# Performance work log

Hardware: AMD Instinct MI355X
Metric: run time of the kernel (lower is better)

The kernel has to match this reference:

```python
import jax, jax.numpy as jnp
import numpy as np

B, T_V, T_T, C, H = 4, 8192, 77, 1024, 16
D = C // H  # head_dim = 64


def setup_inputs() -> dict:
    key = jax.random.key(0)
    ks = jax.random.split(key, 6)
    s = 1.0 / np.sqrt(C)
    return {
        "video_features": jax.random.normal(ks[0], (B, T_V, C), jnp.float32),
        "text_features": jax.random.normal(ks[1], (B, T_T, C), jnp.float32),
        "Wq": jax.random.normal(ks[2], (C, C), jnp.float32) * s,
        "Wk": jax.random.normal(ks[3], (C, C), jnp.float32) * s,
        "Wv": jax.random.normal(ks[4], (C, C), jnp.float32) * s,
        "Wo": jax.random.normal(ks[5], (C, C), jnp.float32) * s,
    }


def reference(video_features, text_features, Wq, Wk, Wv, Wo):
    # nn.Linear(no bias): y = x @ W.T
    q = (video_features @ Wq.T).reshape(B, T_V, H, D).transpose(0, 2, 1, 3)  # [B,H,Tv,D]
    k = (text_features @ Wk.T).reshape(B, T_T, H, D).transpose(0, 2, 1, 3)   # [B,H,Tt,D]
    v = (text_features @ Wv.T).reshape(B, T_T, H, D).transpose(0, 2, 1, 3)   # [B,H,Tt,D]
    scores = jnp.einsum("bhqd,bhkd->bhqk", q, k) / jnp.sqrt(jnp.float32(D))
    attn = jax.nn.softmax(scores, axis=-1)
    out = jnp.einsum("bhqk,bhkd->bhqd", attn, v)
    out = out.transpose(0, 2, 1, 3).reshape(B, T_V, C)
    return out @ Wo.T
```

## Files before the change

kernel.cpp:

```cpp
#include <hip/hip_runtime.h>
#include <hip/hip_bf16.h>


typedef __attribute__((ext_vector_type(8))) short bf16x8;
typedef __attribute__((ext_vector_type(4))) float f32x4;
typedef __attribute__((ext_vector_type(8))) unsigned short u16x8;
typedef __attribute__((ext_vector_type(4))) unsigned short u16x4;

typedef const __attribute__((address_space(1))) void gv_t;
typedef __attribute__((address_space(3))) void lv_t;

static __device__ __forceinline__ unsigned short f2bf(float f) {
    union { float f; unsigned u; } v; v.f = f;
    unsigned r = v.u + 0x7FFFu + ((v.u >> 16) & 1u);
    return (unsigned short)(r >> 16);
}

constexpr int Bn = 4, TVn = 8192, TTn = 77, Cn = 1024, Hn = 16;

__device__ __forceinline__ void cvt8_body(const float* __restrict__ in,
                                          unsigned short* __restrict__ out, int i) {
    const float4* p = reinterpret_cast<const float4*>(in) + (size_t)i * 2;
    float4 a = p[0], b = p[1];
    u16x8 o = { f2bf(a.x), f2bf(a.y), f2bf(a.z), f2bf(a.w),
                f2bf(b.x), f2bf(b.y), f2bf(b.z), f2bf(b.w) };
    *reinterpret_cast<u16x8*>(out + (size_t)i * 8) = o;
}

__global__ __launch_bounds__(256)
void k_prep(const float* __restrict__ video, const float* __restrict__ text,
            const float* __restrict__ Wq, const float* __restrict__ Wk,
            const float* __restrict__ Wv, const float* __restrict__ Wo,
            unsigned short* __restrict__ wq_b, unsigned short* __restrict__ wo_b,
            unsigned short* __restrict__ kbuf, unsigned short* __restrict__ vbuf,
            unsigned short* __restrict__ vid_b) {
    __shared__ unsigned short As[128 * 32];
    __shared__ unsigned short Bs[128 * 32];
    const int tid = threadIdx.x;
    int bid = blockIdx.x;

    if (bid >= 48) {
        bid -= 48;
        if (bid < 512)       cvt8_body(Wq, wq_b, bid * 256 + tid);
        else if (bid < 1024) cvt8_body(Wo, wo_b, (bid - 512) * 256 + tid);
        else                 cvt8_body(video, vid_b, (bid - 1024) * 256 + tid);
        return;
    }
    const int bx = bid % 3, by = (bid / 3) % 8, bz = bid / 24;
    const float* W = bz ? Wv : Wk;
    unsigned short* out = bz ? vbuf : kbuf;
    const int M = Bn * TTn;
    const int lane = tid & 63, wv = tid >> 6;
    const int m0 = bx * 128, n0 = by * 128;
    const int wr = (wv >> 1) * 64, wc = (wv & 1) * 64;
    const int lr = lane & 15, lk = (lane >> 4) * 8, lg = lane >> 4;
    const int srow = tid >> 3, sc4 = (tid & 7) * 4;
    f32x4 acc[4][4] = {};

    float4 a0[4], b0[4], a1[4], b1[4];

#define KV_LOAD(kk, ra, rb)                                                            \
    {                                                                                  \
        _Pragma("unroll")                                                              \
        for (int it = 0; it < 4; ++it) {                                               \
            int row = it * 32 + srow;                                                  \
            int gr = m0 + row;                                                         \
            ra[it] = make_float4(0.f, 0.f, 0.f, 0.f);                                  \
            if (gr < M) ra[it] = *reinterpret_cast<const float4*>(                     \
                text + (size_t)gr * 1024 + (kk) + sc4);                                \
            rb[it] = *reinterpret_cast<const float4*>(                                 \
                W + (size_t)(n0 + row) * 1024 + (kk) + sc4);                           \
        }                                                                              \
    }

#define KV_WRITE(ra, rb)                                                               \
    {                                                                                  \
        _Pragma("unroll")                                                              \
        for (int it = 0; it < 4; ++it) {                                               \
            int row = it * 32 + srow;                                                  \
            u16x4 oa = { f2bf(ra[it].x), f2bf(ra[it].y), f2bf(ra[it].z), f2bf(ra[it].w) }; \
            *reinterpret_cast<u16x4*>(&As[row * 32 + sc4]) = oa;                       \
            u16x4 ob = { f2bf(rb[it].x), f2bf(rb[it].y), f2bf(rb[it].z), f2bf(rb[it].w) }; \
            *reinterpret_cast<u16x4*>(&Bs[row * 32 + sc4]) = ob;                       \
        }                                                                              \
    }

#define KV_COMPUTE()                                                                   \
    {                                                                                  \
        bf16x8 af[4], bfv[4];                                                          \
        _Pragma("unroll")                                                              \
        for (int m = 0; m < 4; ++m)                                                    \
            af[m] = *reinterpret_cast<const bf16x8*>(&As[(wr + m * 16 + lr) * 32 + lk]); \
        _Pragma("unroll")                                                              \
        for (int n = 0; n < 4; ++n)                                                    \
            bfv[n] = *reinterpret_cast<const bf16x8*>(&Bs[(wc + n * 16 + lr) * 32 + lk]); \
        _Pragma("unroll")                                                              \
        for (int m = 0; m < 4; ++m)                                                    \
            _Pragma("unroll")                                                          \
            for (int n = 0; n < 4; ++n)                                                \
                acc[m][n] = __builtin_amdgcn_mfma_f32_16x16x32_bf16(af[m], bfv[n], acc[m][n], 0, 0, 0); \
    }

    KV_LOAD(0, a0, b0);
    for (int kk = 0; kk < 1024; kk += 64) {
        __syncthreads();
        KV_WRITE(a0, b0);
        if (kk + 32 < 1024) KV_LOAD(kk + 32, a1, b1);
        __syncthreads();
        KV_COMPUTE();
        __syncthreads();
        KV_WRITE(a1, b1);
        if (kk + 64 < 1024) KV_LOAD(kk + 64, a0, b0);
        __syncthreads();
        KV_COMPUTE();
    }
#undef KV_LOAD
#undef KV_WRITE
#undef KV_COMPUTE

    #pragma unroll
    for (int m = 0; m < 4; ++m)
        #pragma unroll
        for (int n = 0; n < 4; ++n)
            #pragma unroll
            for (int r = 0; r < 4; ++r) {
                int grow = m0 + wr + m * 16 + lg * 4 + r;
                if (grow < M) {
                    int gcol = n0 + wc + n * 16 + lr;
                    out[(size_t)grow * 1024 + gcol] = f2bf(acc[m][n][r]);
                }
            }
}

__device__ __forceinline__ void stage_h(const unsigned short* __restrict__ src, int grow0, int kcol0,
                                        unsigned short* lds, int tid) {
    #pragma unroll
    for (int j = 0; j < 2; ++j) {
        const int row = j * 64 + (tid >> 3);
        const int sseg = (tid & 7) ^ (row & 7);
        const unsigned short* g = src + (size_t)(grow0 + row) * 1024 + kcol0 + sseg * 8;
        unsigned short* d = lds + j * 4096 + (tid >> 6) * 512;
        __builtin_amdgcn_global_load_lds((gv_t*)g, (lv_t*)d, 16, 0, 0);
    }
}

template<int BUF, int MQ>
__device__ __forceinline__ void p8_loadA(bf16x8 (&af)[4][2],
        const unsigned short (&As)[2][2][128][64], int wm, int lr, int lg) {
    #pragma unroll
    for (int m4 = 0; m4 < 4; ++m4)
        #pragma unroll
        for (int kk = 0; kk < 2; ++kk) {
            const int rl = MQ * 64 + m4 * 16 + lr;
            af[m4][kk] = *reinterpret_cast<const bf16x8*>(
                &As[BUF][wm][rl][((kk * 4 + lg) ^ (rl & 7)) * 8]);
        }
}

template<int BUF, int NQ>
__device__ __forceinline__ void p8_loadB(bf16x8 (&bg)[2][2],
        const unsigned short (&Bs)[2][2][128][64], int wn, int lr, int lg) {
    #pragma unroll
    for (int n2 = 0; n2 < 2; ++n2)
        #pragma unroll
        for (int kk = 0; kk < 2; ++kk) {
            const int nrow = wn * 64 + (NQ * 2 + n2) * 16 + lr;
            bg[n2][kk] = *reinterpret_cast<const bf16x8*>(
                &Bs[BUF][nrow >> 7][nrow & 127][((kk * 4 + lg) ^ (nrow & 7)) * 8]);
        }
}

template<int MQ, int NQ>
__device__ __forceinline__ void p8_mfma(f32x4 (&acc)[8][4],
        const bf16x8 (&af)[4][2], const bf16x8 (&bg)[2][2]) {
    #pragma unroll
    for (int m4 = 0; m4 < 4; ++m4)
        #pragma unroll
        for (int n2 = 0; n2 < 2; ++n2)
            #pragma unroll
            for (int kk = 0; kk < 2; ++kk)
                acc[MQ * 4 + m4][NQ * 2 + n2] = __builtin_amdgcn_mfma_f32_16x16x32_bf16(
                    af[m4][kk], bg[n2][kk], acc[MQ * 4 + m4][NQ * 2 + n2], 0, 0, 0);
}

#define P8_PRE()                                              \
    __builtin_amdgcn_s_barrier();                             \
    __builtin_amdgcn_s_setprio(1);

template<int OUT_MODE>
__global__ __launch_bounds__(512, 1)
void k_g256p8(const unsigned short* __restrict__ A, const unsigned short* __restrict__ Wb,
              void* __restrict__ outp) {
    __shared__ unsigned short As[2][2][128][64];
    __shared__ unsigned short Bs[2][2][128][64];
    const int tid = threadIdx.x, lane = tid & 63;
    const int wid = tid >> 6, wm = wid >> 2, wn = wid & 3;
    const int orig = blockIdx.x;
    const int work = (orig & 7) * 64 + (orig >> 3);
    const int m0 = (work >> 2) * 256, n0 = (work & 3) * 256;
    const int lr = lane & 15, lg = lane >> 4;

    f32x4 acc[8][4] = {};
    bf16x8 af[4][2], bg0[2][2], bg1[2][2];

    stage_h(A,  m0,       0,  &As[0][0][0][0], tid);
    stage_h(A,  m0 + 128, 0,  &As[0][1][0][0], tid);
    stage_h(Wb, n0,       0,  &Bs[0][0][0][0], tid);
    stage_h(Wb, n0 + 128, 0,  &Bs[0][1][0][0], tid);
    stage_h(Wb, n0,       64, &Bs[1][0][0][0], tid);
    stage_h(Wb, n0 + 128, 64, &Bs[1][1][0][0], tid);
    asm volatile("s_waitcnt vmcnt(4)" ::: "memory");
    __builtin_amdgcn_s_barrier();

    for (int t = 0; t < 16; t += 2) {
        const int k1 = (t + 1) * 64;
        const bool s2 = (t + 2) < 16, s3 = (t + 3) < 16;
        p8_loadA<0, 0>(af, As, wm, lr, lg);
        p8_loadB<0, 0>(bg0, Bs, wn, lr, lg);
        stage_h(A, m0, k1, &As[1][0][0][0], tid);
        P8_PRE(); p8_mfma<0, 0>(acc, af, bg0);
        __builtin_amdgcn_s_setprio(0); __builtin_amdgcn_s_barrier();
        p8_loadB<0, 1>(bg1, Bs, wn, lr, lg);
        stage_h(A, m0 + 128, k1, &As[1][1][0][0], tid);
        P8_PRE(); p8_mfma<0, 1>(acc, af, bg1);
        __builtin_amdgcn_s_setprio(0); __builtin_amdgcn_s_barrier();
        p8_loadA<0, 1>(af, As, wm, lr, lg);
        if (s2) stage_h(Wb, n0, k1 + 64, &Bs[0][0][0][0], tid);
        P8_PRE(); p8_mfma<1, 1>(acc, af, bg1);
        __builtin_amdgcn_s_setprio(0); __builtin_amdgcn_s_barrier();
        if (s2) stage_h(Wb, n0 + 128, k1 + 64, &Bs[0][1][0][0], tid);
        P8_PRE(); p8_mfma<1, 0>(acc, af, bg0);
        __builtin_amdgcn_s_setprio(0);
        if (s2) { asm volatile("s_waitcnt vmcnt(4)" ::: "memory"); }
        else    { asm volatile("s_waitcnt vmcnt(0)" ::: "memory"); }
        __builtin_amdgcn_s_barrier();
        p8_loadA<1, 0>(af, As, wm, lr, lg);
        p8_loadB<1, 0>(bg0, Bs, wn, lr, lg);
        if (s2) stage_h(A, m0, k1 + 64, &As[0][0][0][0], tid);
        P8_PRE(); p8_mfma<0, 0>(acc, af, bg0);
        __builtin_amdgcn_s_setprio(0); __builtin_amdgcn_s_barrier();
        p8_loadB<1, 1>(bg1, Bs, wn, lr, lg);
        if (s2) stage_h(A, m0 + 128, k1 + 64, &As[0][1][0][0], tid);
        P8_PRE(); p8_mfma<0, 1>(acc, af, bg1);
        __builtin_amdgcn_s_setprio(0); __builtin_amdgcn_s_barrier();
        p8_loadA<1, 1>(af, As, wm, lr, lg);
        if (s3) stage_h(Wb, n0, k1 + 128, &Bs[1][0][0][0], tid);
        P8_PRE(); p8_mfma<1, 1>(acc, af, bg1);
        __builtin_amdgcn_s_setprio(0); __builtin_amdgcn_s_barrier();
        if (s3) stage_h(Wb, n0 + 128, k1 + 128, &Bs[1][1][0][0], tid);
        P8_PRE(); p8_mfma<1, 0>(acc, af, bg0);
        __builtin_amdgcn_s_setprio(0);
        if (s3) { asm volatile("s_waitcnt vmcnt(4)" ::: "memory"); }
        else    { asm volatile("s_waitcnt vmcnt(0)" ::: "memory"); }
        __builtin_amdgcn_s_barrier();
    }

    #pragma unroll
    for (int mf = 0; mf < 8; ++mf)
        #pragma unroll
        for (int nf = 0; nf < 4; ++nf)
            #pragma unroll
            for (int r = 0; r < 4; ++r) {
                int grow = m0 + wm * 128 + mf * 16 + lg * 4 + r;
                int gcol = n0 + wn * 64 + nf * 16 + lr;
                if (OUT_MODE == 0) {
                    float v = acc[mf][nf][r];
                    float o = __shfl_xor(v, 1);
                    if (!(lane & 1)) {
                        float* out = (float*)outp;
                        float2 pv; pv.x = v; pv.y = o;
                        *reinterpret_cast<float2*>(out + (size_t)grow * 1024 + gcol) = pv;
                    }
                } else {
                    unsigned short bv = f2bf(acc[mf][nf][r]);
                    unsigned ov = __shfl_xor((unsigned)bv, 1);
                    if (!(lane & 1)) {
                        unsigned short* out = (unsigned short*)outp;
                        size_t off = (OUT_MODE == 1)
                            ? (size_t)grow * 1024 + gcol
                            : ((size_t)(gcol >> 6) * (Bn * TVn) + grow) * 64 + (gcol & 63);
                        *reinterpret_cast<unsigned*>(out + off) = (unsigned)bv | (ov << 16);
                    }
                }
            }
}

__global__ __launch_bounds__(512)
void k_attn5(const unsigned short* __restrict__ qh,
             const unsigned short* __restrict__ kb,
             const unsigned short* __restrict__ vb,
             unsigned short* __restrict__ aout) {
    constexpr int VP = 104;
    __shared__ unsigned short vt_s[64 * VP];
    const int tid = threadIdx.x, lane = tid & 63, wv = tid >> 6;
    const int m0 = blockIdx.x * 256;
    const int h = blockIdx.y, b = blockIdx.z;
    const size_t qhbase = ((size_t)h * (Bn * TVn) + (size_t)b * TVn + m0) * 64;
    const size_t kvbase = (size_t)b * TTn * Cn + h * 64;
    const int lr = lane & 15, lg = lane >> 4;

    for (int li = tid; li < 640; li += 512) {
        int t = li >> 3, sg = li & 7;
        u16x8 v = {0, 0, 0, 0, 0, 0, 0, 0};
        if (t < 77) v = *reinterpret_cast<const u16x8*>(vb + kvbase + (size_t)t * Cn + sg * 8);
        #pragma unroll
        for (int i = 0; i < 8; ++i) vt_s[(sg * 8 + i) * VP + t] = v[i];
    }
    for (int li = tid; li < 1024; li += 512) {
        int d = li >> 4, t = 80 + (li & 15);
        vt_s[d * VP + t] = 0;
    }

    f32x4 sc[2][5] = {};
    #pragma unroll
    for (int ks = 0; ks < 2; ++ks) {
        bf16x8 qa[2], kf[5];
        #pragma unroll
        for (int mf = 0; mf < 2; ++mf)
            qa[mf] = *reinterpret_cast<const bf16x8*>(
                qh + qhbase + (size_t)(wv * 32 + mf * 16 + lr) * 64 + ks * 32 + lg * 8);
        #pragma unroll
        for (int nf = 0; nf < 5; ++nf) {
            int t = nf * 16 + lr; if (t > 76) t = 76;
            kf[nf] = *reinterpret_cast<const bf16x8*>(
                kb + kvbase + (size_t)t * Cn + ks * 32 + lg * 8);
        }
        #pragma unroll
        for (int mf = 0; mf < 2; ++mf)
            #pragma unroll
            for (int nf = 0; nf < 5; ++nf)
                sc[mf][nf] = __builtin_amdgcn_mfma_f32_16x16x32_bf16(kf[nf], qa[mf], sc[mf][nf], 0, 0, 0);
    }

    unsigned pk[2][6][2];
    constexpr float CEXP = 0.125f * 1.44269504088896340736f;
    #pragma unroll
    for (int mf = 0; mf < 2; ++mf) {
        float mx = -1e30f;
        #pragma unroll
        for (int nf = 0; nf < 5; ++nf)
            #pragma unroll
            for (int r = 0; r < 4; ++r)
                if (!(nf == 4 && r >= 1)) mx = fmaxf(mx, sc[mf][nf][r]);
                else if (lg != 3)         mx = fmaxf(mx, sc[mf][nf][r]);
        mx = fmaxf(mx, __shfl_xor(mx, 16));
        mx = fmaxf(mx, __shfl_xor(mx, 32));
        float p[5][4];
        float sum = 0.f;
        #pragma unroll
        for (int nf = 0; nf < 5; ++nf)
            #pragma unroll
            for (int r = 0; r < 4; ++r) {
                bool valid = !(nf == 4 && lg == 3 && r >= 1);
                float pv = valid ? exp2f((sc[mf][nf][r] - mx) * CEXP) : 0.f;
                p[nf][r] = pv;
                sum += pv;
            }
        sum += __shfl_xor(sum, 16);
        sum += __shfl_xor(sum, 32);
        float inv = 1.f / sum;
        #pragma unroll
        for (int nf = 0; nf < 5; ++nf) {
            pk[mf][nf][0] = (unsigned)f2bf(p[nf][0] * inv) | ((unsigned)f2bf(p[nf][1] * inv) << 16);
            pk[mf][nf][1] = (unsigned)f2bf(p[nf][2] * inv) | ((unsigned)f2bf(p[nf][3] * inv) << 16);
        }
        pk[mf][5][0] = 0; pk[mf][5][1] = 0;
    }

    __syncthreads();

    f32x4 ovv[2][4] = {};
    const int sel = lg >> 1;
    const int srcA = ((lg & 1) * 2) * 16 + lr;
    const int srcB = ((lg & 1) * 2 + 1) * 16 + lr;
    #pragma unroll
    for (int ks = 0; ks < 3; ++ks) {
        bf16x8 vf[4];
        #pragma unroll
        for (int nf = 0; nf < 4; ++nf)
            vf[nf] = *reinterpret_cast<const bf16x8*>(
                &vt_s[(nf * 16 + lr) * VP + ks * 32 + lg * 8]);
        #pragma unroll
        for (int mf = 0; mf < 2; ++mf) {
            unsigned w0l = __shfl(pk[mf][ks * 2 + 0][0], srcA);
            unsigned w0h = __shfl(pk[mf][ks * 2 + 1][0], srcA);
            unsigned w1l = __shfl(pk[mf][ks * 2 + 0][1], srcA);
            unsigned w1h = __shfl(pk[mf][ks * 2 + 1][1], srcA);
            unsigned w2l = __shfl(pk[mf][ks * 2 + 0][0], srcB);
            unsigned w2h = __shfl(pk[mf][ks * 2 + 1][0], srcB);
            unsigned w3l = __shfl(pk[mf][ks * 2 + 0][1], srcB);
            unsigned w3h = __shfl(pk[mf][ks * 2 + 1][1], srcB);
            union { uint4 u; bf16x8 v; } pa;
            pa.u.x = sel ? w0h : w0l;
            pa.u.y = sel ? w1h : w1l;
            pa.u.z = sel ? w2h : w2l;
            pa.u.w = sel ? w3h : w3l;
            #pragma unroll
            for (int nf = 0; nf < 4; ++nf)
                ovv[mf][nf] = __builtin_amdgcn_mfma_f32_16x16x32_bf16(pa.v, vf[nf], ovv[mf][nf], 0, 0, 0);
        }
    }

    #pragma unroll
    for (int mf = 0; mf < 2; ++mf)
        #pragma unroll
        for (int nf = 0; nf < 4; ++nf)
            #pragma unroll
            for (int r = 0; r < 4; ++r) {
                unsigned short bv = f2bf(ovv[mf][nf][r]);
                unsigned o = __shfl_xor((unsigned)bv, 1);
                if (!(lane & 1)) {
                    int row = m0 + wv * 32 + mf * 16 + lg * 4 + r;
                    int col = h * 64 + nf * 16 + lr;
                    *reinterpret_cast<unsigned*>(aout + ((size_t)b * TVn + row) * Cn + col) =
                        (unsigned)bv | (o << 16);
                }
            }
}

extern "C" void kernel_launch(void* const* d_in, const int* in_sizes, int n_in,
                              void* d_out, int out_size, void* d_ws, size_t ws_size,
                              hipStream_t stream) {
    const float* video = (const float*)d_in[0];
    const float* text  = (const float*)d_in[1];
    const float* Wq = (const float*)d_in[2];
    const float* Wk = (const float*)d_in[3];
    const float* Wv = (const float*)d_in[4];
    const float* Wo = (const float*)d_in[5];
    float* out = (float*)d_out;

    char* ws = (char*)d_ws;
    unsigned short* wq_b  = (unsigned short*)(ws);
    unsigned short* wo_b  = (unsigned short*)(ws + (2u << 20));
    unsigned short* kbuf  = (unsigned short*)(ws + (4u << 20));
    unsigned short* vbuf  = (unsigned short*)(ws + (5u << 20));
    unsigned short* qhbuf = (unsigned short*)(ws + (6u << 20));
    unsigned short* vid_b = (unsigned short*)(ws + (70u << 20));

    k_prep<<<48 + 512 + 512 + 16384, 256, 0, stream>>>(
        video, text, Wq, Wk, Wv, Wo, wq_b, wo_b, kbuf, vbuf, vid_b);

    k_g256p8<2><<<512, 512, 0, stream>>>(vid_b, wq_b, (void*)qhbuf);

    dim3 ga(TVn / 256, Hn, Bn);
    k_attn5<<<ga, 512, 0, stream>>>(qhbuf, kbuf, vbuf, vid_b);

    k_g256p8<0><<<512, 512, 0, stream>>>(vid_b, wo_b, (void*)out);
}
```

Baseline: 255.4 us.

## Fuse video fp32-to-bf16 conversion into Q projection GEMM A-operand load

Removes the separate conversion of video features to bf16 in the prep kernel and instead loads fp32 video tiles directly in a new Q-projection GEMM, converting to bf16 in registers before writing to LDS with an XOR swizzle. This eliminates writing and rereading a large bf16 intermediate buffer. In exchange, the GEMM reads twice the bytes per A tile (fp32), repeated across the N-tile blocks, and holds extra prefetch registers.

```diff
diff --git a/kernel.cpp b/kernel.cpp
--- a/kernel.cpp
+++ b/kernel.cpp
@@ -28,12 +28,11 @@
 }
 
 __global__ __launch_bounds__(256)
-void k_prep(const float* __restrict__ video, const float* __restrict__ text,
+void k_prep(const float* __restrict__ text,
             const float* __restrict__ Wq, const float* __restrict__ Wk,
             const float* __restrict__ Wv, const float* __restrict__ Wo,
             unsigned short* __restrict__ wq_b, unsigned short* __restrict__ wo_b,
-            unsigned short* __restrict__ kbuf, unsigned short* __restrict__ vbuf,
-            unsigned short* __restrict__ vid_b) {
+            unsigned short* __restrict__ kbuf, unsigned short* __restrict__ vbuf) {
     __shared__ unsigned short As[128 * 32];
     __shared__ unsigned short Bs[128 * 32];
     const int tid = threadIdx.x;
@@ -41,9 +40,8 @@
 
     if (bid >= 48) {
         bid -= 48;
-        if (bid < 512)       cvt8_body(Wq, wq_b, bid * 256 + tid);
-        else if (bid < 1024) cvt8_body(Wo, wo_b, (bid - 512) * 256 + tid);
-        else                 cvt8_body(video, vid_b, (bid - 1024) * 256 + tid);
+        if (bid < 512) cvt8_body(Wq, wq_b, bid * 256 + tid);
+        else           cvt8_body(Wo, wo_b, (bid - 512) * 256 + tid);
         return;
     }
     const int bx = bid % 3, by = (bid / 3) % 8, bz = bid / 24;
@@ -186,6 +184,120 @@
 #define P8_PRE()                                              \
     __builtin_amdgcn_s_barrier();                             \
     __builtin_amdgcn_s_setprio(1);
+
+__global__ __launch_bounds__(512, 1)
+void k_gq_fused(const float* __restrict__ A, const unsigned short* __restrict__ Wb,
+                unsigned short* __restrict__ outp) {
+    __shared__ unsigned short As[2][2][128][64];
+    __shared__ unsigned short Bs[2][2][128][64];
+    const int tid = threadIdx.x, lane = tid & 63;
+    const int wid = tid >> 6, wm = wid >> 2, wn = wid & 3;
+    const int orig = blockIdx.x;
+    const int work = (orig & 7) * 64 + (orig >> 3);
+    const int m0 = (work >> 2) * 256, n0 = (work & 3) * 256;
+    const int lr = lane & 15, lg = lane >> 4;
+    const int srow = tid >> 3, sw = tid & 7, sa = (tid & 7) ^ ((tid >> 3) & 7);
+
+    f32x4 acc[8][4] = {};
+    bf16x8 af[4][2], bg0[2][2], bg1[2][2];
+    float4 ra0[2][2][2], ra1[2][2][2];
+
+#define AQ_LOAD(bank, kt)                                                          \
+    { const int kc_ = (kt) * 64;                                                   \
+      _Pragma("unroll") for (int hh = 0; hh < 2; ++hh)                             \
+      _Pragma("unroll") for (int j = 0; j < 2; ++j) {                              \
+          const float* g_ = A + (size_t)(m0 + hh * 128 + j * 64 + srow) * 1024 + kc_ + sa * 8; \
+          bank[hh][j][0] = *reinterpret_cast<const float4*>(g_);                   \
+          bank[hh][j][1] = *reinterpret_cast<const float4*>(g_ + 4);               \
+      } }
+
+#define AQ_WRITE(bank, BUF, HH)                                                    \
+    { _Pragma("unroll") for (int j = 0; j < 2; ++j) {                              \
+          float4 u_ = bank[HH][j][0], v_ = bank[HH][j][1];                         \
+          u16x8 o_ = { f2bf(u_.x), f2bf(u_.y), f2bf(u_.z), f2bf(u_.w),             \
+                       f2bf(v_.x), f2bf(v_.y), f2bf(v_.z), f2bf(v_.w) };           \
+          *reinterpret_cast<u16x8*>(&As[BUF][HH][j * 64 + srow][sw * 8]) = o_;     \
+      } }
+
+    AQ_LOAD(ra0, 0);
+    AQ_LOAD(ra1, 1);
+    stage_h(Wb, n0,       0,  &Bs[0][0][0][0], tid);
+    stage_h(Wb, n0 + 128, 0,  &Bs[0][1][0][0], tid);
+    stage_h(Wb, n0,       64, &Bs[1][0][0][0], tid);
+    stage_h(Wb, n0 + 128, 64, &Bs[1][1][0][0], tid);
+    AQ_WRITE(ra0, 0, 0);
+    AQ_WRITE(ra0, 0, 1);
+    asm volatile("s_waitcnt vmcnt(4)" ::: "memory");
+    asm volatile("s_waitcnt lgkmcnt(0)" ::: "memory");
+    __builtin_amdgcn_s_barrier();
+
+    for (int t = 0; t < 16; t += 2) {
+        const int k1 = (t + 1) * 64;
+        const bool s2 = (t + 2) < 16, s3 = (t + 3) < 16;
+        p8_loadA<0, 0>(af, As, wm, lr, lg);
+        p8_loadB<0, 0>(bg0, Bs, wn, lr, lg);
+        AQ_WRITE(ra1, 1, 0);
+        if (s2) AQ_LOAD(ra0, t + 2);
+        P8_PRE(); p8_mfma<0, 0>(acc, af, bg0);
+        __builtin_amdgcn_s_setprio(0); __builtin_amdgcn_s_barrier();
+        p8_loadB<0, 1>(bg1, Bs, wn, lr, lg);
+        AQ_WRITE(ra1, 1, 1);
+        P8_PRE(); p8_mfma<0, 1>(acc, af, bg1);
+        __builtin_amdgcn_s_setprio(0);
+        asm volatile("s_waitcnt lgkmcnt(0)" ::: "memory");
+        __builtin_amdgcn_s_barrier();
+        p8_loadA<0, 1>(af, As, wm, lr, lg);
+        if (s2) stage_h(Wb, n0, k1 + 64, &Bs[0][0][0][0], tid);
+        P8_PRE(); p8_mfma<1, 1>(acc, af, bg1);
+        __builtin_amdgcn_s_setprio(0); __builtin_amdgcn_s_barrier();
+        if (s2) stage_h(Wb, n0 + 128, k1 + 64, &Bs[0][1][0][0], tid);
+        P8_PRE(); p8_mfma<1, 0>(acc, af, bg0);
+        __builtin_amdgcn_s_setprio(0);
+        if (s2) { asm volatile("s_waitcnt vmcnt(4)" ::: "memory"); }
+        else    { asm volatile("s_waitcnt vmcnt(0)" ::: "memory"); }
+        __builtin_amdgcn_s_barrier();
+        p8_loadA<1, 0>(af, As, wm, lr, lg);
+        p8_loadB<1, 0>(bg0, Bs, wn, lr, lg);
+        if (s2) AQ_WRITE(ra0, 0, 0);
+        if (s3) AQ_LOAD(ra1, t + 3);
+        P8_PRE(); p8_mfma<0, 0>(acc, af, bg0);
+        __builtin_amdgcn_s_setprio(0); __builtin_amdgcn_s_barrier();
+        p8_loadB<1, 1>(bg1, Bs, wn, lr, lg);
+        if (s2) AQ_WRITE(ra0, 0, 1);
+        P8_PRE(); p8_mfma<0, 1>(acc, af, bg1);
+        __builtin_amdgcn_s_setprio(0);
+        asm volatile("s_waitcnt lgkmcnt(0)" ::: "memory");
+        __builtin_amdgcn_s_barrier();
+        p8_loadA<1, 1>(af, As, wm, lr, lg);
+        if (s3) stage_h(Wb, n0, k1 + 128, &Bs[1][0][0][0], tid);
+        P8_PRE(); p8_mfma<1, 1>(acc, af, bg1);
+        __builtin_amdgcn_s_setprio(0); __builtin_amdgcn_s_barrier();
+        if (s3) stage_h(Wb, n0 + 128, k1 + 128, &Bs[1][1][0][0], tid);
+        P8_PRE(); p8_mfma<1, 0>(acc, af, bg0);
+        __builtin_amdgcn_s_setprio(0);
+        if (s3) { asm volatile("s_waitcnt vmcnt(4)" ::: "memory"); }
+        else    { asm volatile("s_waitcnt vmcnt(0)" ::: "memory"); }
+        __builtin_amdgcn_s_barrier();
+    }
+#undef AQ_LOAD
+#undef AQ_WRITE
+
+    #pragma unroll
+    for (int mf = 0; mf < 8; ++mf)
+        #pragma unroll
+        for (int nf = 0; nf < 4; ++nf)
+            #pragma unroll
+            for (int r = 0; r < 4; ++r) {
+                int grow = m0 + wm * 128 + mf * 16 + lg * 4 + r;
+                int gcol = n0 + wn * 64 + nf * 16 + lr;
+                unsigned short bv = f2bf(acc[mf][nf][r]);
+                unsigned ov = __shfl_xor((unsigned)bv, 1);
+                if (!(lane & 1)) {
+                    size_t off = ((size_t)(gcol >> 6) * (Bn * TVn) + grow) * 64 + (gcol & 63);
+                    *reinterpret_cast<unsigned*>(outp + off) = (unsigned)bv | (ov << 16);
+                }
+            }
+}
 
 template<int OUT_MODE>
 __global__ __launch_bounds__(512, 1)
@@ -435,15 +547,15 @@
     unsigned short* kbuf  = (unsigned short*)(ws + (4u << 20));
     unsigned short* vbuf  = (unsigned short*)(ws + (5u << 20));
     unsigned short* qhbuf = (unsigned short*)(ws + (6u << 20));
-    unsigned short* vid_b = (unsigned short*)(ws + (70u << 20));
-
-    k_prep<<<48 + 512 + 512 + 16384, 256, 0, stream>>>(
-        video, text, Wq, Wk, Wv, Wo, wq_b, wo_b, kbuf, vbuf, vid_b);
-
-    k_g256p8<2><<<512, 512, 0, stream>>>(vid_b, wq_b, (void*)qhbuf);
+    unsigned short* abuf  = (unsigned short*)(ws + (70u << 20));
+
+    k_prep<<<48 + 512 + 512, 256, 0, stream>>>(
+        text, Wq, Wk, Wv, Wo, wq_b, wo_b, kbuf, vbuf);
+
+    k_gq_fused<<<512, 512, 0, stream>>>(video, wq_b, qhbuf);
 
     dim3 ga(TVn / 256, Hn, Bn);
-    k_attn5<<<ga, 512, 0, stream>>>(qhbuf, kbuf, vbuf, vid_b);
-
-    k_g256p8<0><<<512, 512, 0, stream>>>(vid_b, wo_b, (void*)out);
-}
+    k_attn5<<<ga, 512, 0, stream>>>(qhbuf, kbuf, vbuf, abuf);
+
+    k_g256p8<0><<<512, 512, 0, stream>>>(abuf, wo_b, (void*)out);
+}
```

Measured after the change: 516.9 us. 2.02x slower.
